# Kernel tuning notes

Measured on AMD Instinct MI355X. Metric: run time of the kernel, lower is better.

The kernel has to match this reference:

```python
import jax, jax.numpy as jnp
import numpy as np

H, CH = 4, 16          # heads, hidden_features // heads
SLOPE = 0.2            # leaky_relu negative slope


def gat(x, W, a_src, a_dst):
    # x: (B, N, C); W: (hidden, C); a_src/a_dst: (H, CH)
    B, N, _ = x.shape
    h = (x @ W.T).reshape(B, N, H, CH)
    a1 = jnp.einsum('bnhc,hc->bnh', h, a_src)   # att_src scores
    a2 = jnp.einsum('bnhc,hc->bnh', h, a_dst)   # att_dst scores
    # torch: a1.unsqueeze(1) + a2.unsqueeze(2) -> (B, N, N, H)
    e = a1[:, None, :, :] + a2[:, :, None, :]
    e = jnp.transpose(e, (0, 3, 1, 2))          # (B, H, N, N)
    e = jnp.where(e >= 0, e, SLOPE * e)         # leaky_relu
    return jax.nn.softmax(e, axis=2)            # softmax over dim=2 as in torch


def pool(x, W1, b1, W2, b2):
    # diff-pool assignment: (B, N, K), then x' = S^T x -> (B, K, C)
    s = jax.nn.softmax(jax.nn.relu(x @ W1.T + b1) @ W2.T + b2, axis=-1)
    return jnp.einsum('bnk,bnc->bkc', s, x)


def fuse(att0, atts, lefts, rights):
    out = att0
    for a, l, r in zip(atts, lefts, rights):
        # left (H,J0,K) @ att (B,H,K,K) @ right (H,K,J0), broadcast over batch
        out = out + jnp.einsum('hjk,bhkl,hlm->bhjm', l, a, r)
    return out


def setup_inputs() -> dict:
    key = jax.random.key(0)
    ks = iter(jax.random.split(key, 40))
    n = lambda shape, s=0.1: jax.random.normal(next(ks), shape, dtype=jnp.float32) * s
    inp = {
        'src': n((64, 64, 64, 25), 1.0),
        'gat_lin': n((6, 64, 64)), 'gat_asrc': n((6, 4, 16)), 'gat_adst': n((6, 4, 16)),
        'sp0_W1': n((64, 64)), 'sp0_b1': jnp.zeros((64,), jnp.float32),
        'sp0_W2': n((12, 64)), 'sp0_b2': jnp.zeros((12,), jnp.float32),
        'sp1_W1': n((64, 64)), 'sp1_b1': jnp.zeros((64,), jnp.float32),
        'sp1_W2': n((5, 64)), 'sp1_b2': jnp.zeros((5,), jnp.float32),
        'tp0_W1': n((64, 64)), 'tp0_b1': jnp.zeros((64,), jnp.float32),
        'tp0_W2': n((32, 64)), 'tp0_b2': jnp.zeros((32,), jnp.float32),
        'tp1_W1': n((64, 64)), 'tp1_b1': jnp.zeros((64,), jnp.float32),
        'tp1_W2': n((12, 64)), 'tp1_b2': jnp.zeros((12,), jnp.float32),
        'sl0': n((4, 25, 12)), 'sr0': n((4, 12, 25)),
        'sl1': n((4, 25, 5)), 'sr1': n((4, 5, 25)),
        'tl0': n((4, 64, 32)), 'tr0': n((4, 32, 64)),
        'tl1': n((4, 64, 12)), 'tr1': n((4, 12, 64)),
    }
    return inp


def reference(src, gat_lin, gat_asrc, gat_adst,
              sp0_W1, sp0_b1, sp0_W2, sp0_b2, sp1_W1, sp1_b1, sp1_W2, sp1_b2,
              tp0_W1, tp0_b1, tp0_W2, tp0_b2, tp1_W1, tp1_b1, tp1_W2, tp1_b2,
              sl0, sr0, sl1, sr1, tl0, tr0, tl1, tr1):
    B, C, T, J = src.shape
    # ---- spatial branch: attention over joints per (batch, frame) ----
    xs = jnp.transpose(src, (0, 2, 3, 1)).reshape(B * T, J, C)
    a_s0 = gat(xs, gat_lin[0], gat_asrc[0], gat_adst[0])            # (BT,H,25,25)
    xs1 = pool(xs, sp0_W1, sp0_b1, sp0_W2, sp0_b2)                  # (BT,12,C)
    a_s1 = gat(xs1, gat_lin[1], gat_asrc[1], gat_adst[1])           # (BT,H,12,12)
    xs2 = pool(xs1, sp1_W1, sp1_b1, sp1_W2, sp1_b2)                 # (BT,5,C)
    a_s2 = gat(xs2, gat_lin[2], gat_asrc[2], gat_adst[2])           # (BT,H,5,5)
    s_fused = fuse(a_s0, [a_s1, a_s2], [sl0, sl1], [sr0, sr1])
    # ---- temporal branch: attention over frames per (batch, joint) ----
    xt = jnp.transpose(src, (0, 3, 2, 1)).reshape(B * J, T, C)
    a_t0 = gat(xt, gat_lin[3], gat_asrc[3], gat_adst[3])            # (BJ,H,64,64)
    xt1 = pool(xt, tp0_W1, tp0_b1, tp0_W2, tp0_b2)                  # (BJ,32,C)
    a_t1 = gat(xt1, gat_lin[4], gat_asrc[4], gat_adst[4])
    xt2 = pool(xt1, tp1_W1, tp1_b1, tp1_W2, tp1_b2)                 # (BJ,12,C)
    a_t2 = gat(xt2, gat_lin[5], gat_asrc[5], gat_adst[5])
    t_fused = fuse(a_t0, [a_t1, a_t2], [tl0, tl1], [tr0, tr1])
    return (s_fused.reshape(B, T, H, J, J), t_fused.reshape(B, J, H, T, T))
```

## Files before the change

### kernel.cpp

```cpp
#include <hip/hip_runtime.h>

#define DEVINL __device__ __forceinline__

DEVINL float leaky(float v) { return v >= 0.f ? v : 0.2f * v; }

__global__ void wprep_kernel(const float* __restrict__ lin,
                             const float* __restrict__ asrc,
                             const float* __restrict__ adst,
                             float* __restrict__ w_out) {
    int idx = blockIdx.x * blockDim.x + threadIdx.x;
    if (idx >= 6 * 4 * 64) return;
    int c = idx & 63;
    int h = (idx >> 6) & 3;
    int k = idx >> 8;
    const float* L = lin + k * 64 * 64;
    float s1 = 0.f, s2 = 0.f;
    for (int e = 0; e < 16; ++e) {
        float w = L[(h * 16 + e) * 64 + c];
        s1 += w * asrc[(k * 4 + h) * 16 + e];
        s2 += w * adst[(k * 4 + h) * 16 + e];
    }
    w_out[(k * 2 + 0) * 256 + h * 64 + c] = s1;
    w_out[(k * 2 + 1) * 256 + h * 64 + c] = s2;
}

__global__ void wtrans_kernel(const float* __restrict__ s0, const float* __restrict__ s1,
                              const float* __restrict__ t0, const float* __restrict__ t1,
                              const float* __restrict__ s0w2, const float* __restrict__ s1w2,
                              const float* __restrict__ t0w2, const float* __restrict__ t1w2,
                              float* __restrict__ o) {
    int idx = blockIdx.x * 256 + threadIdx.x;
    if (idx < 16384) {
        int m = idx >> 12, r = idx & 4095, c = r >> 6, d = r & 63;
        const float* src = (m == 0) ? s0 : (m == 1) ? s1 : (m == 2) ? t0 : t1;
        o[idx] = src[d * 64 + c];
    } else if (idx < 16384 + 768) {
        int j = idx - 16384, c = j / 12, k = j - 12 * c;
        o[idx] = s0w2[k * 64 + c];
    } else if (idx < 17152 + 512) {
        int j = idx - 17152, c = j >> 3, k = j & 7;
        o[idx] = (k < 5) ? s1w2[k * 64 + c] : 0.f;
    } else if (idx < 17664 + 2048) {
        int j = idx - 17664, c = j >> 5, k = j & 31;
        o[idx] = t0w2[k * 64 + c];
    } else if (idx < 19712 + 768) {
        int j = idx - 19712, c = j / 12, k = j - 12 * c;
        o[idx] = t1w2[k * 64 + c];
    }
}

__global__ void xs_kernel(const float* __restrict__ src, float* __restrict__ xs) {
    int g = blockIdx.x;
    int b = g >> 6, t = g & 63;
    __shared__ float tile[64][26];
    const float* sp = src + b * 102400 + t * 25;
    for (int idx = threadIdx.x; idx < 64 * 25; idx += blockDim.x) {
        int c = idx / 25, j = idx - c * 25;
        tile[c][j] = sp[c * 1600 + j];
    }
    __syncthreads();
    float* op = xs + g * 25 * 64;
    for (int idx = threadIdx.x; idx < 25 * 64; idx += blockDim.x) {
        int j = idx >> 6, c = idx & 63;
        op[idx] = tile[c][j];
    }
}

__global__ void xt_kernel(const float* __restrict__ src, float* __restrict__ xt) {
    int g = blockIdx.x;
    int b = g / 25, j = g - b * 25;
    __shared__ float tile[64][65];
    const float* sp = src + b * 102400 + j;
    for (int idx = threadIdx.x; idx < 64 * 64; idx += blockDim.x) {
        int c = idx >> 6, t = idx & 63;
        tile[c][t] = sp[c * 1600 + t * 25];
    }
    __syncthreads();
    float* op = xt + g * 64 * 64;
    for (int idx = threadIdx.x; idx < 64 * 64; idx += blockDim.x) {
        int t = idx >> 6, c = idx & 63;
        op[idx] = tile[c][t];
    }
}

template <int N, int GPB>
__global__ __launch_bounds__(256) void score_kernel(
    const float* __restrict__ x,
    const float* __restrict__ w,
    float* __restrict__ sc) {
    constexpr int NP = GPB * N;
    constexpr int LD = NP + 1;
    __shared__ float xlT[64 * LD];
    __shared__ float wl[512];
    const int g0 = blockIdx.x * GPB;
    const int tid = threadIdx.x;
    const float* xp = x + (size_t)g0 * N * 64;
    for (int idx = tid; idx < NP * 64; idx += 256) {
        int n = idx >> 6, c = idx & 63;
        xlT[c * LD + n] = xp[idx];
    }
    for (int idx = tid; idx < 512; idx += 256) wl[idx] = w[idx];
    __syncthreads();
    float* op = sc + (size_t)g0 * 8 * N;
    for (int idx = tid; idx < 8 * NP; idx += 256) {
        int n = idx % N;
        int q = (idx / N) & 7;
        int gs = idx / (8 * N);
        int nn = gs * N + n;
        const float* wp = wl + q * 64;
        float acc = 0.f;
        #pragma unroll 8
        for (int c = 0; c < 64; ++c) acc += xlT[c * LD + nn] * wp[c];
        op[idx] = acc;
    }
}

template <int N, int K, int KP>
__global__ __launch_bounds__(256, 3) void pool_kernel(
    const float* __restrict__ x,
    const float* __restrict__ W1T,
    const float* __restrict__ b1,
    const float* __restrict__ W2T,
    const float* __restrict__ b2,
    float* __restrict__ xo) {
    constexpr int NP = (N + 3) & ~3;
    constexpr int LDN = NP + 1;
    __shared__ float xlT[64 * LDN];
    __shared__ float yT[64 * LDN];
    __shared__ float sT[KP * LDN];
    const int g = blockIdx.x, tid = threadIdx.x;
    const float* xp = x + (size_t)g * N * 64;
    for (int i4 = tid; i4 < N * 16; i4 += 256) {
        int n = i4 >> 4, c0 = (i4 & 15) << 2;
        float4 v = ((const float4*)xp)[i4];
        xlT[(c0 + 0) * LDN + n] = v.x;
        xlT[(c0 + 1) * LDN + n] = v.y;
        xlT[(c0 + 2) * LDN + n] = v.z;
        xlT[(c0 + 3) * LDN + n] = v.w;
    }
    if constexpr (NP > N) {
        for (int i = tid; i < 64 * (NP - N); i += 256) {
            int c = i / (NP - N), n = N + i % (NP - N);
            xlT[c * LDN + n] = 0.f;
        }
    }
    __syncthreads();
    constexpr int T1 = (NP / 4) * 16;
    if (tid < T1) {
        int d0 = (tid & 15) << 2, n0 = (tid >> 4) << 2;
        float acc[4][4] = {};
        #pragma unroll 4
        for (int c = 0; c < 64; ++c) {
            float4 w4 = *(const float4*)(W1T + c * 64 + d0);
            float wv[4] = {w4.x, w4.y, w4.z, w4.w};
            float xv[4];
            #pragma unroll
            for (int r = 0; r < 4; ++r) xv[r] = xlT[c * LDN + n0 + r];
            #pragma unroll
            for (int r = 0; r < 4; ++r)
                #pragma unroll
                for (int cc = 0; cc < 4; ++cc) acc[r][cc] += xv[r] * wv[cc];
        }
        float4 b4 = *(const float4*)(b1 + d0);
        float bb[4] = {b4.x, b4.y, b4.z, b4.w};
        #pragma unroll
        for (int r = 0; r < 4; ++r)
            #pragma unroll
            for (int cc = 0; cc < 4; ++cc)
                yT[(d0 + cc) * LDN + n0 + r] = fmaxf(acc[r][cc] + bb[cc], 0.f);
    }
    __syncthreads();
    constexpr int KG4 = KP / 4;
    constexpr int T2 = (NP / 4) * KG4;
    if (tid < T2) {
        int k0 = (tid % KG4) << 2, n0 = (tid / KG4) << 2;
        float acc[4][4] = {};
        #pragma unroll 4
        for (int d = 0; d < 64; ++d) {
            float4 w4 = *(const float4*)(W2T + d * KP + k0);
            float wv[4] = {w4.x, w4.y, w4.z, w4.w};
            float yv[4];
            #pragma unroll
            for (int r = 0; r < 4; ++r) yv[r] = yT[d * LDN + n0 + r];
            #pragma unroll
            for (int r = 0; r < 4; ++r)
                #pragma unroll
                for (int cc = 0; cc < 4; ++cc) acc[r][cc] += yv[r] * wv[cc];
        }
        #pragma unroll
        for (int cc = 0; cc < 4; ++cc) {
            int k = k0 + cc;
            float bb = (k < K) ? b2[k] : 0.f;
            #pragma unroll
            for (int r = 0; r < 4; ++r)
                sT[k * LDN + n0 + r] = (k < K) ? (acc[r][cc] + bb) : -1e30f;
        }
    }
    __syncthreads();
    if (tid < NP) {
        float m = -1e30f;
        #pragma unroll
        for (int k = 0; k < KP; ++k) m = fmaxf(m, sT[k * LDN + tid]);
        float sum = 0.f;
        float e[KP];
        #pragma unroll
        for (int k = 0; k < KP; ++k) { e[k] = __expf(sT[k * LDN + tid] - m); sum += e[k]; }
        float inv = 1.f / sum;
        #pragma unroll
        for (int k = 0; k < KP; ++k) sT[k * LDN + tid] = e[k] * inv;
    }
    __syncthreads();
    constexpr int KG2 = (K + 1) / 2;
    constexpr int T3 = KG2 * 16;
    if (tid < T3) {
        int k0 = (tid % KG2) * 2, c0 = (tid / KG2) * 4;
        float acc0[4] = {}, acc1[4] = {};
        #pragma unroll 4
        for (int n = 0; n < N; ++n) {
            float sv0 = sT[k0 * LDN + n];
            float sv1 = sT[(k0 + 1) * LDN + n];
            float xv[4];
            #pragma unroll
            for (int j = 0; j < 4; ++j) xv[j] = xlT[(c0 + j) * LDN + n];
            #pragma unroll
            for (int j = 0; j < 4; ++j) { acc0[j] += sv0 * xv[j]; acc1[j] += sv1 * xv[j]; }
        }
        float* op = xo + (size_t)g * K * 64;
        *(float4*)&op[k0 * 64 + c0] = make_float4(acc0[0], acc0[1], acc0[2], acc0[3]);
        if (k0 + 1 < K)
            *(float4*)&op[(k0 + 1) * 64 + c0] = make_float4(acc1[0], acc1[1], acc1[2], acc1[3]);
    }
}

__global__ __launch_bounds__(256, 8) void gatfuse_t(
    const float* __restrict__ sc0,
    const float* __restrict__ sc1,
    const float* __restrict__ sc2,
    const float* __restrict__ L1,
    const float* __restrict__ R1,
    const float* __restrict__ L2,
    const float* __restrict__ R2,
    float* __restrict__ out)
{
    const int bid = blockIdx.x;
    const int g = (bid & 7) | ((bid >> 5) << 3);
    const int h = (bid >> 3) & 3;
    const int tid = threadIdx.x;
    __shared__ float t1T[32 * 64];
    __shared__ float t2T[12 * 64];
    __shared__ float A1[32 * 36];
    __shared__ float A2[12 * 13];
    __shared__ float a01[64], a02[64], mj0[64], iv0[64];
    __shared__ float a11[32], a12[32], mj1[32], iv1[32];
    __shared__ float a21[12], a22[12], mj2[12], iv2[12];

    if (tid < 128) {
        int t = tid & 63, sd = tid >> 6;
        (sd ? a02 : a01)[t] = sc0[((size_t)g * 8 + sd * 4 + h) * 64 + t];
    } else if (tid < 192) {
        int u = tid - 128, sd = u >> 5, n = u & 31;
        (sd ? a12 : a11)[n] = sc1[((size_t)g * 8 + sd * 4 + h) * 32 + n];
    } else if (tid < 216) {
        int u = tid - 192, sd = u / 12, n = u - sd * 12;
        (sd ? a22 : a21)[n] = sc2[((size_t)g * 8 + sd * 4 + h) * 12 + n];
    }
    __syncthreads();

    if (tid < 64) {
        float mx = a02[0];
        for (int i = 1; i < 64; ++i) mx = fmaxf(mx, a02[i]);
        float aj = a01[tid];
        float mj = leaky(aj + mx);
        float s = 0.f;
        for (int i = 0; i < 64; ++i) s += __expf(leaky(aj + a02[i]) - mj);
        mj0[tid] = mj; iv0[tid] = 1.f / s;
    } else if (tid < 96) {
        int l = tid - 64;
        float mx = a12[0];
        for (int k = 1; k < 32; ++k) mx = fmaxf(mx, a12[k]);
        float aj = a11[l];
        float mj = leaky(aj + mx);
        float s = 0.f;
        for (int k = 0; k < 32; ++k) s += __expf(leaky(aj + a12[k]) - mj);
        mj1[l] = mj; iv1[l] = 1.f / s;
    } else if (tid < 108) {
        int l = tid - 96;
        float mx = a22[0];
        for (int k = 1; k < 12; ++k) mx = fmaxf(mx, a22[k]);
        float aj = a21[l];
        float mj = leaky(aj + mx);
        float s = 0.f;
        for (int k = 0; k < 12; ++k) s += __expf(leaky(aj + a22[k]) - mj);
        mj2[l] = mj; iv2[l] = 1.f / s;
    }
    __syncthreads();

    #pragma unroll
    for (int q = 0; q < 4; ++q) {
        int idx = q * 256 + tid;
        int k = idx >> 5, l = idx & 31;
        float e = leaky(a11[l] + a12[k]);
        A1[k * 36 + l] = __expf(e - mj1[l]) * iv1[l];
    }
    if (tid < 144) {
        int k = tid / 12, l = tid - k * 12;
        float e = leaky(a21[l] + a22[k]);
        A2[k * 13 + l] = __expf(e - mj2[l]) * iv2[l];
    }
    __syncthreads();

    {
        const int j = tid & 63, l0 = (tid >> 6) * 8;
        const float* ljrow = L1 + ((size_t)h * 64 + j) * 32;
        float acc8[8] = {};
        for (int k = 0; k < 32; ++k) {
            float lk = ljrow[k];
            float4 a4a = *(const float4*)&A1[k * 36 + l0];
            float4 a4b = *(const float4*)&A1[k * 36 + l0 + 4];
            acc8[0] += lk * a4a.x; acc8[1] += lk * a4a.y;
            acc8[2] += lk * a4a.z; acc8[3] += lk * a4a.w;
            acc8[4] += lk * a4b.x; acc8[5] += lk * a4b.y;
            acc8[6] += lk * a4b.z; acc8[7] += lk * a4b.w;
        }
        #pragma unroll
        for (int lo = 0; lo < 8; ++lo) t1T[(l0 + lo) * 64 + j] = acc8[lo];
        const int lb = (tid >> 6) * 3;
        float lj2[12];
        const float4* lp2 = (const float4*)(L2 + ((size_t)h * 64 + j) * 12);
        #pragma unroll
        for (int q = 0; q < 3; ++q) {
            float4 v = lp2[q];
            lj2[q * 4] = v.x; lj2[q * 4 + 1] = v.y;
            lj2[q * 4 + 2] = v.z; lj2[q * 4 + 3] = v.w;
        }
        #pragma unroll
        for (int lo = 0; lo < 3; ++lo) {
            int l = lb + lo;
            float acc = 0.f;
            #pragma unroll
            for (int k = 0; k < 12; ++k) acc += lj2[k] * A2[k * 13 + l];
            t2T[l * 64 + j] = acc;
        }
    }
    __syncthreads();

    const int i0 = (tid >> 4) << 2, m0 = (tid & 15) << 2;
    float acc[4][4];
    {
        float4 q1 = *(const float4*)&a01[m0];
        float4 qm = *(const float4*)&mj0[m0];
        float4 qv = *(const float4*)&iv0[m0];
        float4 q2 = *(const float4*)&a02[i0];
        float am[4] = {q1.x, q1.y, q1.z, q1.w};
        float mv[4] = {qm.x, qm.y, qm.z, qm.w};
        float iv[4] = {qv.x, qv.y, qv.z, qv.w};
        float ai[4] = {q2.x, q2.y, q2.z, q2.w};
        #pragma unroll
        for (int r = 0; r < 4; ++r)
            #pragma unroll
            for (int c = 0; c < 4; ++c) {
                float e = am[c] + ai[r];
                e = e >= 0.f ? e : 0.2f * e;
                acc[r][c] = __expf(e - mv[c]) * iv[c];
            }
    }
    const float* r1b = R1 + (size_t)h * 2048;
    #pragma unroll 8
    for (int l = 0; l < 32; ++l) {
        float4 t4 = *(const float4*)&t1T[l * 64 + i0];
        float4 r4 = *(const float4*)(r1b + l * 64 + m0);
        float tv[4] = {t4.x, t4.y, t4.z, t4.w};
        float rv[4] = {r4.x, r4.y, r4.z, r4.w};
        #pragma unroll
        for (int r = 0; r < 4; ++r)
            #pragma unroll
            for (int c = 0; c < 4; ++c) acc[r][c] += tv[r] * rv[c];
    }
    const float* r2b = R2 + (size_t)h * 768;
    #pragma unroll 4
    for (int l = 0; l < 12; ++l) {
        float4 t4 = *(const float4*)&t2T[l * 64 + i0];
        float4 r4 = *(const float4*)(r2b + l * 64 + m0);
        float tv[4] = {t4.x, t4.y, t4.z, t4.w};
        float rv[4] = {r4.x, r4.y, r4.z, r4.w};
        #pragma unroll
        for (int r = 0; r < 4; ++r)
            #pragma unroll
            for (int c = 0; c < 4; ++c) acc[r][c] += tv[r] * rv[c];
    }
    float* op = out + ((size_t)g * 4 + h) * 4096;
    #pragma unroll
    for (int r = 0; r < 4; ++r)
        *(float4*)&op[(i0 + r) * 64 + m0] =
            make_float4(acc[r][0], acc[r][1], acc[r][2], acc[r][3]);
}

__global__ __launch_bounds__(256, 6) void gatfuse_s(
    const float* __restrict__ sc0,
    const float* __restrict__ sc1,
    const float* __restrict__ sc2,
    const float* __restrict__ L1,
    const float* __restrict__ R1,
    const float* __restrict__ L2,
    const float* __restrict__ R2,
    float* __restrict__ out)
{
    const int g = blockIdx.x;
    const int tid = threadIdx.x;
    const int h = tid >> 6, t = tid & 63;
    __shared__ float A1[4][12 * 13];
    __shared__ float A2[4][5 * 6];
    __shared__ float t1l[4][25 * 16];
    __shared__ float t2l[4][25 * 8];
    __shared__ float r1T[4][25 * 16];
    __shared__ float r2T[4][25 * 8];
    __shared__ float a01[4][25], a02[4][25], mj0[4][25], iv0[4][25];
    __shared__ float a11[4][12], a12[4][12], mj1[4][12], iv1[4][12];
    __shared__ float a21[4][5], a22[4][5], mj2[4][5], iv2[4][5];

    if (t < 50) {
        int sd = t / 25, n = t - sd * 25;
        (sd ? a02[h] : a01[h])[n] = sc0[((size_t)g * 8 + sd * 4 + h) * 25 + n];
    }
    if (t < 24) {
        int sd = t / 12, n = t - sd * 12;
        (sd ? a12[h] : a11[h])[n] = sc1[((size_t)g * 8 + sd * 4 + h) * 12 + n];
    }
    if (t < 10) {
        int sd = t / 5, n = t - sd * 5;
        (sd ? a22[h] : a21[h])[n] = sc2[((size_t)g * 8 + sd * 4 + h) * 5 + n];
    }
    for (int idx = t; idx < 400; idx += 64) {
        int m = idx >> 4, l = idx & 15;
        r1T[h][idx] = (l < 12) ? R1[h * 300 + l * 25 + m] : 0.f;
    }
    for (int idx = t; idx < 200; idx += 64) {
        int m = idx >> 3, l = idx & 7;
        r2T[h][idx] = (l < 5) ? R2[h * 125 + l * 25 + m] : 0.f;
    }
    __syncthreads();

    if (t < 25) {
        float mx = a02[h][0];
        for (int i = 1; i < 25; ++i) mx = fmaxf(mx, a02[h][i]);
        float aj = a01[h][t];
        float mj = leaky(aj + mx);
        float s = 0.f;
        for (int i = 0; i < 25; ++i) s += __expf(leaky(aj + a02[h][i]) - mj);
        mj0[h][t] = mj; iv0[h][t] = 1.f / s;
    }
    if (t >= 32 && t < 44) {
        int l = t - 32;
        float mx = a12[h][0];
        for (int k = 1; k < 12; ++k) mx = fmaxf(mx, a12[h][k]);
        float aj = a11[h][l];
        float mj = leaky(aj + mx);
        float s = 0.f;
        for (int k = 0; k < 12; ++k) s += __expf(leaky(aj + a12[h][k]) - mj);
        mj1[h][l] = mj; iv1[h][l] = 1.f / s;
    }
    if (t >= 48 && t < 53) {
        int l = t - 48;
        float mx = a22[h][0];
        for (int k = 1; k < 5; ++k) mx = fmaxf(mx, a22[h][k]);
        float aj = a21[h][l];
        float mj = leaky(aj + mx);
        float s = 0.f;
        for (int k = 0; k < 5; ++k) s += __expf(leaky(aj + a22[h][k]) - mj);
        mj2[h][l] = mj; iv2[h][l] = 1.f / s;
    }
    __syncthreads();

    for (int idx = t; idx < 144; idx += 64) {
        int k = idx / 12, l = idx - k * 12;
        float e = leaky(a11[h][l] + a12[h][k]);
        A1[h][k * 13 + l] = __expf(e - mj1[h][l]) * iv1[h][l];
    }
    if (t < 25) {
        int k = t / 5, l = t - (t / 5) * 5;
        float e = leaky(a21[h][l] + a22[h][k]);
        A2[h][k * 6 + l] = __expf(e - mj2[h][l]) * iv2[h][l];
    }
    __syncthreads();

    if (t < 25) {
        float lj[12];
        const float4* lp = (const float4*)(L1 + ((size_t)h * 25 + t) * 12);
        #pragma unroll
        for (int q = 0; q < 3; ++q) {
            float4 v = lp[q];
            lj[q * 4] = v.x; lj[q * 4 + 1] = v.y; lj[q * 4 + 2] = v.z; lj[q * 4 + 3] = v.w;
        }
        #pragma unroll
        for (int l = 0; l < 12; ++l) {
            float acc = 0.f;
            #pragma unroll
            for (int k = 0; k < 12; ++k) acc += lj[k] * A1[h][k * 13 + l];
            t1l[h][t * 16 + l] = acc;
        }
        #pragma unroll
        for (int l = 12; l < 16; ++l) t1l[h][t * 16 + l] = 0.f;
        float lj2[5];
        const float* lp2 = L2 + ((size_t)h * 25 + t) * 5;
        #pragma unroll
        for (int k = 0; k < 5; ++k) lj2[k] = lp2[k];
        #pragma unroll
        for (int l = 0; l < 5; ++l) {
            float acc = 0.f;
            #pragma unroll
            for (int k = 0; k < 5; ++k) acc += lj2[k] * A2[h][k * 6 + l];
            t2l[h][t * 8 + l] = acc;
        }
        #pragma unroll
        for (int l = 5; l < 8; ++l) t2l[h][t * 8 + l] = 0.f;
    }
    __syncthreads();

    float* op = out + ((size_t)g * 4 + h) * 625;
    for (int idx = t; idx < 625; idx += 64) {
        int i = idx / 25, m = idx - i * 25;
        float e = a01[h][m] + a02[h][i];
        e = e >= 0.f ? e : 0.2f * e;
        float val = __expf(e - mj0[h][m]) * iv0[h][m];
        const float* t1r = &t1l[h][i * 16];
        const float* r1c = &r1T[h][m * 16];
        #pragma unroll
        for (int q = 0; q < 4; ++q) {
            float4 tv = *(const float4*)&t1r[q * 4];
            float4 rv = *(const float4*)&r1c[q * 4];
            val += tv.x * rv.x + tv.y * rv.y + tv.z * rv.z + tv.w * rv.w;
        }
        const float* t2r = &t2l[h][i * 8];
        const float* r2c = &r2T[h][m * 8];
        #pragma unroll
        for (int q = 0; q < 2; ++q) {
            float4 tv = *(const float4*)&t2r[q * 4];
            float4 rv = *(const float4*)&r2c[q * 4];
            val += tv.x * rv.x + tv.y * rv.y + tv.z * rv.z + tv.w * rv.w;
        }
        op[idx] = val;
    }
}

extern "C" void kernel_launch(void* const* d_in, const int* in_sizes, int n_in,
                              void* d_out, int out_size, void* d_ws, size_t ws_size,
                              hipStream_t stream) {
    const float* src    = (const float*)d_in[0];
    const float* lin    = (const float*)d_in[1];
    const float* asrc   = (const float*)d_in[2];
    const float* adst   = (const float*)d_in[3];
    const float* sp0_W1 = (const float*)d_in[4];
    const float* sp0_b1 = (const float*)d_in[5];
    const float* sp0_W2 = (const float*)d_in[6];
    const float* sp0_b2 = (const float*)d_in[7];
    const float* sp1_W1 = (const float*)d_in[8];
    const float* sp1_b1 = (const float*)d_in[9];
    const float* sp1_W2 = (const float*)d_in[10];
    const float* sp1_b2 = (const float*)d_in[11];
    const float* tp0_W1 = (const float*)d_in[12];
    const float* tp0_b1 = (const float*)d_in[13];
    const float* tp0_W2 = (const float*)d_in[14];
    const float* tp0_b2 = (const float*)d_in[15];
    const float* tp1_W1 = (const float*)d_in[16];
    const float* tp1_b1 = (const float*)d_in[17];
    const float* tp1_W2 = (const float*)d_in[18];
    const float* tp1_b2 = (const float*)d_in[19];
    const float* sl0    = (const float*)d_in[20];
    const float* sr0    = (const float*)d_in[21];
    const float* sl1    = (const float*)d_in[22];
    const float* sr1    = (const float*)d_in[23];
    const float* tl0    = (const float*)d_in[24];
    const float* tr0    = (const float*)d_in[25];
    const float* tl1    = (const float*)d_in[26];
    const float* tr1    = (const float*)d_in[27];

    float* out_s = (float*)d_out;
    float* out_t = out_s + 10240000;

    float* ws   = (float*)d_ws;
    float* wbuf = ws;
    float* wT   = ws + 4096;
    float* base = ws + 24576;

    float* sp0_W1T = wT;
    float* sp1_W1T = wT + 4096;
    float* tp0_W1T = wT + 8192;
    float* tp1_W1T = wT + 12288;
    float* sp0_W2T = wT + 16384;
    float* sp1_W2T = wT + 17152;
    float* tp0_W2T = wT + 17664;
    float* tp1_W2T = wT + 19712;

    float* xs  = base;
    float* xs1 = base + 6553600;
    float* xs2 = base + 9699328;
    float* xt  = base;
    float* xt1 = base + 6553600;
    float* xt2 = base + 9830400;
    float* scb = base + 11059200;
    float* scS0 = scb;
    float* scS1 = scb + 819200;
    float* scS2 = scb + 1212416;
    float* scT0 = scb;
    float* scT1 = scb + 819200;
    float* scT2 = scb + 1228800;

    wprep_kernel<<<6, 256, 0, stream>>>(lin, asrc, adst, wbuf);
    wtrans_kernel<<<80, 256, 0, stream>>>(sp0_W1, sp1_W1, tp0_W1, tp1_W1,
                                          sp0_W2, sp1_W2, tp0_W2, tp1_W2, wT);

    xs_kernel<<<4096, 256, 0, stream>>>(src, xs);
    score_kernel<25, 2><<<2048, 256, 0, stream>>>(xs, wbuf + 0 * 512, scS0);
    pool_kernel<25, 12, 12><<<4096, 256, 0, stream>>>(xs, sp0_W1T, sp0_b1, sp0_W2T, sp0_b2, xs1);
    score_kernel<12, 4><<<1024, 256, 0, stream>>>(xs1, wbuf + 1 * 512, scS1);
    pool_kernel<12, 5, 8><<<4096, 256, 0, stream>>>(xs1, sp1_W1T, sp1_b1, sp1_W2T, sp1_b2, xs2);
    score_kernel<5, 8><<<512, 256, 0, stream>>>(xs2, wbuf + 2 * 512, scS2);
    gatfuse_s<<<4096, 256, 0, stream>>>(scS0, scS1, scS2, sl0, sr0, sl1, sr1, out_s);

    xt_kernel<<<1600, 256, 0, stream>>>(src, xt);
    score_kernel<64, 1><<<1600, 256, 0, stream>>>(xt, wbuf + 3 * 512, scT0);
    pool_kernel<64, 32, 32><<<1600, 256, 0, stream>>>(xt, tp0_W1T, tp0_b1, tp0_W2T, tp0_b2, xt1);
    score_kernel<32, 2><<<800, 256, 0, stream>>>(xt1, wbuf + 4 * 512, scT1);
    pool_kernel<32, 12, 12><<<1600, 256, 0, stream>>>(xt1, tp1_W1T, tp1_b1, tp1_W2T, tp1_b2, xt2);
    score_kernel<12, 4><<<400, 256, 0, stream>>>(xt2, wbuf + 5 * 512, scT2);
    gatfuse_t<<<6400, 256, 0, stream>>>(scT0, scT1, scT2, tl0, tr0, tl1, tr1, out_t);
}
```

Before: 386.8 us.

## Fuse transpose, score and pooling kernels; factor leaky softmax into separable exponentials

The input transposes (xs/xt) and the per-level attention score kernels are folded into the pooling kernel. Each pool launch now reads src directly, computes the input-level and output-level scores, and writes the pooled features only when the next level needs them. This cuts the launch count from 14 to 6 and removes the round trips of xs/xt/xs2/xt2 through global memory. In the gatfuse kernels, the leaky-relu softmax is rewritten as products of precomputed per-row and per-column exponentials selected by the sign of the sum, replacing the per-element exp. That adds LDS and register pressure and drops the launch-bounds occupancy hint.

```diff
diff --git a/kernel.cpp b/kernel.cpp
--- a/kernel.cpp
+++ b/kernel.cpp
@@ -49,186 +49,167 @@
     }
 }
 
-__global__ void xs_kernel(const float* __restrict__ src, float* __restrict__ xs) {
-    int g = blockIdx.x;
-    int b = g >> 6, t = g & 63;
-    __shared__ float tile[64][26];
-    const float* sp = src + b * 102400 + t * 25;
-    for (int idx = threadIdx.x; idx < 64 * 25; idx += blockDim.x) {
-        int c = idx / 25, j = idx - c * 25;
-        tile[c][j] = sp[c * 1600 + j];
-    }
-    __syncthreads();
-    float* op = xs + g * 25 * 64;
-    for (int idx = threadIdx.x; idx < 25 * 64; idx += blockDim.x) {
-        int j = idx >> 6, c = idx & 63;
-        op[idx] = tile[c][j];
-    }
-}
-
-__global__ void xt_kernel(const float* __restrict__ src, float* __restrict__ xt) {
-    int g = blockIdx.x;
-    int b = g / 25, j = g - b * 25;
-    __shared__ float tile[64][65];
-    const float* sp = src + b * 102400 + j;
-    for (int idx = threadIdx.x; idx < 64 * 64; idx += blockDim.x) {
-        int c = idx >> 6, t = idx & 63;
-        tile[c][t] = sp[c * 1600 + t * 25];
-    }
-    __syncthreads();
-    float* op = xt + g * 64 * 64;
-    for (int idx = threadIdx.x; idx < 64 * 64; idx += blockDim.x) {
-        int t = idx >> 6, c = idx & 63;
-        op[idx] = tile[c][t];
-    }
-}
-
-template <int N, int GPB>
-__global__ __launch_bounds__(256) void score_kernel(
-    const float* __restrict__ x,
-    const float* __restrict__ w,
-    float* __restrict__ sc) {
-    constexpr int NP = GPB * N;
-    constexpr int LD = NP + 1;
-    __shared__ float xlT[64 * LD];
-    __shared__ float wl[512];
-    const int g0 = blockIdx.x * GPB;
-    const int tid = threadIdx.x;
-    const float* xp = x + (size_t)g0 * N * 64;
-    for (int idx = tid; idx < NP * 64; idx += 256) {
-        int n = idx >> 6, c = idx & 63;
-        xlT[c * LD + n] = xp[idx];
-    }
-    for (int idx = tid; idx < 512; idx += 256) wl[idx] = w[idx];
-    __syncthreads();
-    float* op = sc + (size_t)g0 * 8 * N;
-    for (int idx = tid; idx < 8 * NP; idx += 256) {
-        int n = idx % N;
-        int q = (idx / N) & 7;
-        int gs = idx / (8 * N);
-        int nn = gs * N + n;
-        const float* wp = wl + q * 64;
+template <int N, int K, int KP, int MODE, int WR>
+__global__ __launch_bounds__(256) void pool_kernel(
+    const float* __restrict__ x, const float* __restrict__ W1T,
+    const float* __restrict__ b1, const float* __restrict__ W2T,
+    const float* __restrict__ b2, const float* __restrict__ wsi,
+    const float* __restrict__ wso, float* __restrict__ xo,
+    float* __restrict__ sci, float* __restrict__ sco)
+{
+    constexpr int SLD = KP + 1;
+    constexpr int XO_OFF = ((N * SLD + 3) & ~3);
+    constexpr int SZT = (MODE == 1) ? 64 * 26 : (MODE == 2 ? 64 * 65 : 0);
+    constexpr int R3A = XO_OFF + K * 68;
+    constexpr int R3 = ((R3A > SZT ? R3A : SZT) + 3) & ~3;
+    constexpr int TOT = 2 * N * 68 + R3 + 512;
+    __shared__ float lds[TOT];
+    float* xln = lds;
+    float* yn  = lds + N * 68;
+    float* r3  = yn + N * 68;
+    float* sn  = r3;
+    float* xoL = r3 + XO_OFF;
+    float* wlo = r3 + R3;
+    float* wli = yn;
+    float* tile = r3;
+    const int g = blockIdx.x, tid = threadIdx.x;
+
+    if constexpr (MODE == 0) {
+        const float4* xp = (const float4*)(x + (size_t)g * N * 64);
+        for (int p = tid; p < N * 16; p += 256) {
+            int n = p >> 4, c0 = (p & 15) << 2;
+            *(float4*)&xln[n * 68 + c0] = xp[p];
+        }
+    } else if constexpr (MODE == 1) {
+        int b = g >> 6, t = g & 63;
+        const float* sp = x + b * 102400 + t * 25;
+        for (int idx = tid; idx < 1600; idx += 256) {
+            int c = idx / 25, j = idx - c * 25;
+            tile[c * 26 + j] = sp[c * 1600 + j];
+        }
+        for (int i = tid; i < 512; i += 256) wli[i] = wsi[i];
+    } else {
+        int b = g / 25, j = g - b * 25;
+        const float* sp = x + b * 102400 + j;
+        for (int idx = tid; idx < 4096; idx += 256) {
+            int c = idx >> 6, t = idx & 63;
+            tile[c * 65 + t] = sp[c * 1600 + t * 25];
+        }
+        for (int i = tid; i < 512; i += 256) wli[i] = wsi[i];
+    }
+    for (int i = tid; i < 512; i += 256) wlo[i] = wso[i];
+    __syncthreads();
+
+    if constexpr (MODE != 0) {
+        constexpr int TLD = (MODE == 1) ? 26 : 65;
+        for (int p = tid; p < N * 64; p += 256) {
+            int n = p >> 6, c = p & 63;
+            xln[n * 68 + c] = tile[c * TLD + n];
+        }
+        __syncthreads();
+        for (int p = tid; p < 8 * N; p += 256) {
+            int q = p / N, n = p - q * N;
+            const float* wv = wli + q * 64;
+            const float* xr = &xln[n * 68];
+            float acc = 0.f;
+            #pragma unroll
+            for (int c0 = 0; c0 < 64; c0 += 4) {
+                float4 xv = *(const float4*)&xr[c0];
+                float4 w4 = *(const float4*)&wv[c0];
+                acc += xv.x * w4.x + xv.y * w4.y + xv.z * w4.z + xv.w * w4.w;
+            }
+            sci[(size_t)g * 8 * N + p] = acc;
+        }
+        __syncthreads();
+    }
+
+    for (int p = tid; p < N * 16; p += 256) {
+        int n = p >> 4, d0 = (p & 15) << 2;
+        const float* xr = &xln[n * 68];
+        float4 bb = *(const float4*)(b1 + d0);
+        float a0 = bb.x, a1 = bb.y, a2 = bb.z, a3 = bb.w;
+        #pragma unroll 4
+        for (int c0 = 0; c0 < 64; c0 += 4) {
+            float4 xv = *(const float4*)&xr[c0];
+            float4 w0 = *(const float4*)(W1T + (c0 + 0) * 64 + d0);
+            float4 w1 = *(const float4*)(W1T + (c0 + 1) * 64 + d0);
+            float4 w2 = *(const float4*)(W1T + (c0 + 2) * 64 + d0);
+            float4 w3 = *(const float4*)(W1T + (c0 + 3) * 64 + d0);
+            a0 += xv.x * w0.x + xv.y * w1.x + xv.z * w2.x + xv.w * w3.x;
+            a1 += xv.x * w0.y + xv.y * w1.y + xv.z * w2.y + xv.w * w3.y;
+            a2 += xv.x * w0.z + xv.y * w1.z + xv.z * w2.z + xv.w * w3.z;
+            a3 += xv.x * w0.w + xv.y * w1.w + xv.z * w2.w + xv.w * w3.w;
+        }
+        *(float4*)&yn[n * 68 + d0] =
+            make_float4(fmaxf(a0, 0.f), fmaxf(a1, 0.f), fmaxf(a2, 0.f), fmaxf(a3, 0.f));
+    }
+    __syncthreads();
+
+    for (int p = tid; p < N * (KP / 4); p += 256) {
+        int n = p / (KP / 4), k0 = (p % (KP / 4)) << 2;
+        const float* yr = &yn[n * 68];
+        float a0 = 0.f, a1 = 0.f, a2 = 0.f, a3 = 0.f;
+        #pragma unroll 4
+        for (int d0 = 0; d0 < 64; d0 += 4) {
+            float4 yv = *(const float4*)&yr[d0];
+            float4 w0 = *(const float4*)(W2T + (d0 + 0) * KP + k0);
+            float4 w1 = *(const float4*)(W2T + (d0 + 1) * KP + k0);
+            float4 w2 = *(const float4*)(W2T + (d0 + 2) * KP + k0);
+            float4 w3 = *(const float4*)(W2T + (d0 + 3) * KP + k0);
+            a0 += yv.x * w0.x + yv.y * w1.x + yv.z * w2.x + yv.w * w3.x;
+            a1 += yv.x * w0.y + yv.y * w1.y + yv.z * w2.y + yv.w * w3.y;
+            a2 += yv.x * w0.z + yv.y * w1.z + yv.z * w2.z + yv.w * w3.z;
+            a3 += yv.x * w0.w + yv.y * w1.w + yv.z * w2.w + yv.w * w3.w;
+        }
+        float* sr = &sn[n * SLD + k0];
+        sr[0] = (k0 + 0 < K) ? a0 + b2[k0 + 0] : -1e30f;
+        sr[1] = (k0 + 1 < K) ? a1 + b2[k0 + 1] : -1e30f;
+        sr[2] = (k0 + 2 < K) ? a2 + b2[k0 + 2] : -1e30f;
+        sr[3] = (k0 + 3 < K) ? a3 + b2[k0 + 3] : -1e30f;
+    }
+    __syncthreads();
+
+    if (tid < N) {
+        float* sr = &sn[tid * SLD];
+        float m = sr[0];
+        #pragma unroll
+        for (int k = 1; k < KP; ++k) m = fmaxf(m, sr[k]);
+        float sum = 0.f;
+        #pragma unroll
+        for (int k = 0; k < KP; ++k) { float e = __expf(sr[k] - m); sr[k] = e; sum += e; }
+        float inv = 1.f / sum;
+        #pragma unroll
+        for (int k = 0; k < KP; ++k) sr[k] *= inv;
+    }
+    __syncthreads();
+
+    for (int p = tid; p < K * 16; p += 256) {
+        int k = p >> 4, c0 = (p & 15) << 2;
+        float a0 = 0.f, a1 = 0.f, a2 = 0.f, a3 = 0.f;
+        for (int n = 0; n < N; ++n) {
+            float s = sn[n * SLD + k];
+            float4 xv = *(const float4*)&xln[n * 68 + c0];
+            a0 += s * xv.x; a1 += s * xv.y; a2 += s * xv.z; a3 += s * xv.w;
+        }
+        float4 r = make_float4(a0, a1, a2, a3);
+        *(float4*)&xoL[k * 68 + c0] = r;
+        if constexpr (WR)
+            *(float4*)(xo + (size_t)g * K * 64 + k * 64 + c0) = r;
+    }
+    __syncthreads();
+
+    for (int p = tid; p < 8 * K; p += 256) {
+        int q = p / K, k = p - q * K;
+        const float* wv = wlo + q * 64;
+        const float* xr = &xoL[k * 68];
         float acc = 0.f;
-        #pragma unroll 8
-        for (int c = 0; c < 64; ++c) acc += xlT[c * LD + nn] * wp[c];
-        op[idx] = acc;
-    }
-}
-
-template <int N, int K, int KP>
-__global__ __launch_bounds__(256, 3) void pool_kernel(
-    const float* __restrict__ x,
-    const float* __restrict__ W1T,
-    const float* __restrict__ b1,
-    const float* __restrict__ W2T,
-    const float* __restrict__ b2,
-    float* __restrict__ xo) {
-    constexpr int NP = (N + 3) & ~3;
-    constexpr int LDN = NP + 1;
-    __shared__ float xlT[64 * LDN];
-    __shared__ float yT[64 * LDN];
-    __shared__ float sT[KP * LDN];
-    const int g = blockIdx.x, tid = threadIdx.x;
-    const float* xp = x + (size_t)g * N * 64;
-    for (int i4 = tid; i4 < N * 16; i4 += 256) {
-        int n = i4 >> 4, c0 = (i4 & 15) << 2;
-        float4 v = ((const float4*)xp)[i4];
-        xlT[(c0 + 0) * LDN + n] = v.x;
-        xlT[(c0 + 1) * LDN + n] = v.y;
-        xlT[(c0 + 2) * LDN + n] = v.z;
-        xlT[(c0 + 3) * LDN + n] = v.w;
-    }
-    if constexpr (NP > N) {
-        for (int i = tid; i < 64 * (NP - N); i += 256) {
-            int c = i / (NP - N), n = N + i % (NP - N);
-            xlT[c * LDN + n] = 0.f;
-        }
-    }
-    __syncthreads();
-    constexpr int T1 = (NP / 4) * 16;
-    if (tid < T1) {
-        int d0 = (tid & 15) << 2, n0 = (tid >> 4) << 2;
-        float acc[4][4] = {};
-        #pragma unroll 4
-        for (int c = 0; c < 64; ++c) {
-            float4 w4 = *(const float4*)(W1T + c * 64 + d0);
-            float wv[4] = {w4.x, w4.y, w4.z, w4.w};
-            float xv[4];
-            #pragma unroll
-            for (int r = 0; r < 4; ++r) xv[r] = xlT[c * LDN + n0 + r];
-            #pragma unroll
-            for (int r = 0; r < 4; ++r)
-                #pragma unroll
-                for (int cc = 0; cc < 4; ++cc) acc[r][cc] += xv[r] * wv[cc];
-        }
-        float4 b4 = *(const float4*)(b1 + d0);
-        float bb[4] = {b4.x, b4.y, b4.z, b4.w};
-        #pragma unroll
-        for (int r = 0; r < 4; ++r)
-            #pragma unroll
-            for (int cc = 0; cc < 4; ++cc)
-                yT[(d0 + cc) * LDN + n0 + r] = fmaxf(acc[r][cc] + bb[cc], 0.f);
-    }
-    __syncthreads();
-    constexpr int KG4 = KP / 4;
-    constexpr int T2 = (NP / 4) * KG4;
-    if (tid < T2) {
-        int k0 = (tid % KG4) << 2, n0 = (tid / KG4) << 2;
-        float acc[4][4] = {};
-        #pragma unroll 4
-        for (int d = 0; d < 64; ++d) {
-            float4 w4 = *(const float4*)(W2T + d * KP + k0);
-            float wv[4] = {w4.x, w4.y, w4.z, w4.w};
-            float yv[4];
-            #pragma unroll
-            for (int r = 0; r < 4; ++r) yv[r] = yT[d * LDN + n0 + r];
-            #pragma unroll
-            for (int r = 0; r < 4; ++r)
-                #pragma unroll
-                for (int cc = 0; cc < 4; ++cc) acc[r][cc] += yv[r] * wv[cc];
-        }
-        #pragma unroll
-        for (int cc = 0; cc < 4; ++cc) {
-            int k = k0 + cc;
-            float bb = (k < K) ? b2[k] : 0.f;
-            #pragma unroll
-            for (int r = 0; r < 4; ++r)
-                sT[k * LDN + n0 + r] = (k < K) ? (acc[r][cc] + bb) : -1e30f;
-        }
-    }
-    __syncthreads();
-    if (tid < NP) {
-        float m = -1e30f;
-        #pragma unroll
-        for (int k = 0; k < KP; ++k) m = fmaxf(m, sT[k * LDN + tid]);
-        float sum = 0.f;
-        float e[KP];
-        #pragma unroll
-        for (int k = 0; k < KP; ++k) { e[k] = __expf(sT[k * LDN + tid] - m); sum += e[k]; }
-        float inv = 1.f / sum;
-        #pragma unroll
-        for (int k = 0; k < KP; ++k) sT[k * LDN + tid] = e[k] * inv;
-    }
-    __syncthreads();
-    constexpr int KG2 = (K + 1) / 2;
-    constexpr int T3 = KG2 * 16;
-    if (tid < T3) {
-        int k0 = (tid % KG2) * 2, c0 = (tid / KG2) * 4;
-        float acc0[4] = {}, acc1[4] = {};
-        #pragma unroll 4
-        for (int n = 0; n < N; ++n) {
-            float sv0 = sT[k0 * LDN + n];
-            float sv1 = sT[(k0 + 1) * LDN + n];
-            float xv[4];
-            #pragma unroll
-            for (int j = 0; j < 4; ++j) xv[j] = xlT[(c0 + j) * LDN + n];
-            #pragma unroll
-            for (int j = 0; j < 4; ++j) { acc0[j] += sv0 * xv[j]; acc1[j] += sv1 * xv[j]; }
-        }
-        float* op = xo + (size_t)g * K * 64;
-        *(float4*)&op[k0 * 64 + c0] = make_float4(acc0[0], acc0[1], acc0[2], acc0[3]);
-        if (k0 + 1 < K)
-            *(float4*)&op[(k0 + 1) * 64 + c0] = make_float4(acc1[0], acc1[1], acc1[2], acc1[3]);
+        #pragma unroll
+        for (int c0 = 0; c0 < 64; c0 += 4) {
+            float4 xv = *(const float4*)&xr[c0];
+            float4 w4 = *(const float4*)&wv[c0];
+            acc += xv.x * w4.x + xv.y * w4.y + xv.z * w4.z + xv.w * w4.w;
+        }
+        sco[(size_t)g * 8 * K + p] = acc;
     }
 }
 
@@ -250,48 +231,84 @@
     __shared__ float t2T[12 * 64];
     __shared__ float A1[32 * 36];
     __shared__ float A2[12 * 13];
-    __shared__ float a01[64], a02[64], mj0[64], iv0[64];
-    __shared__ float a11[32], a12[32], mj1[32], iv1[32];
-    __shared__ float a21[12], a22[12], mj2[12], iv2[12];
-
-    if (tid < 128) {
-        int t = tid & 63, sd = tid >> 6;
-        (sd ? a02 : a01)[t] = sc0[((size_t)g * 8 + sd * 4 + h) * 64 + t];
-    } else if (tid < 192) {
-        int u = tid - 128, sd = u >> 5, n = u & 31;
-        (sd ? a12 : a11)[n] = sc1[((size_t)g * 8 + sd * 4 + h) * 32 + n];
-    } else if (tid < 216) {
-        int u = tid - 192, sd = u / 12, n = u - sd * 12;
-        (sd ? a22 : a21)[n] = sc2[((size_t)g * 8 + sd * 4 + h) * 12 + n];
-    }
+    __shared__ float4 row0[64], col0[64], row1[32], col1[32], row2[12], col2[12];
+    __shared__ float mxs[3];
+
+    if (tid < 64) col0[tid].x = sc0[((size_t)g * 8 + h) * 64 + tid];
+    else if (tid < 128) row0[tid - 64].x = sc0[((size_t)g * 8 + 4 + h) * 64 + (tid - 64)];
+    else if (tid < 160) col1[tid - 128].x = sc1[((size_t)g * 8 + h) * 32 + (tid - 128)];
+    else if (tid < 192) row1[tid - 160].x = sc1[((size_t)g * 8 + 4 + h) * 32 + (tid - 160)];
+    else if (tid < 204) col2[tid - 192].x = sc2[((size_t)g * 8 + h) * 12 + (tid - 192)];
+    else if (tid < 216) row2[tid - 204].x = sc2[((size_t)g * 8 + 4 + h) * 12 + (tid - 204)];
     __syncthreads();
 
     if (tid < 64) {
-        float mx = a02[0];
-        for (int i = 1; i < 64; ++i) mx = fmaxf(mx, a02[i]);
-        float aj = a01[tid];
-        float mj = leaky(aj + mx);
-        float s = 0.f;
-        for (int i = 0; i < 64; ++i) s += __expf(leaky(aj + a02[i]) - mj);
-        mj0[tid] = mj; iv0[tid] = 1.f / s;
+        float mx = row0[0].x;
+        for (int i = 1; i < 64; ++i) mx = fmaxf(mx, row0[i].x);
+        if (tid == 0) mxs[0] = mx;
+        float a = row0[tid].x;
+        row0[tid] = make_float4(a, __expf(a - mx), __expf(0.2f * (a - mx)), 0.f);
+    } else if (tid < 96) {
+        float mx = row1[0].x;
+        for (int k = 1; k < 32; ++k) mx = fmaxf(mx, row1[k].x);
+        if (tid == 64) mxs[1] = mx;
+        int k = tid - 64;
+        float a = row1[k].x;
+        row1[k] = make_float4(a, __expf(a - mx), __expf(0.2f * (a - mx)), 0.f);
+    } else if (tid < 108) {
+        float mx = row2[0].x;
+        for (int k = 1; k < 12; ++k) mx = fmaxf(mx, row2[k].x);
+        if (tid == 96) mxs[2] = mx;
+        int k = tid - 96;
+        float a = row2[k].x;
+        row2[k] = make_float4(a, __expf(a - mx), __expf(0.2f * (a - mx)), 0.f);
+    }
+    __syncthreads();
+
+    if (tid < 64) {
+        float a = col0[tid].x, mx = mxs[0];
+        float mj = leaky(a + mx);
+        float Em = __expf(a + mx - mj);
+        float Fm = __expf(0.2f * (a + mx) - mj);
+        float S1 = 0.f, S2 = 0.f;
+        for (int i = 0; i < 64; ++i) {
+            float4 r = row0[i];
+            bool c = (a + r.x >= 0.f);
+            S1 += c ? r.y : 0.f;
+            S2 += c ? 0.f : r.z;
+        }
+        float iv = 1.f / (Em * S1 + Fm * S2);
+        col0[tid] = make_float4(a, Em * iv, Fm * iv, 0.f);
     } else if (tid < 96) {
         int l = tid - 64;
-        float mx = a12[0];
-        for (int k = 1; k < 32; ++k) mx = fmaxf(mx, a12[k]);
-        float aj = a11[l];
-        float mj = leaky(aj + mx);
-        float s = 0.f;
-        for (int k = 0; k < 32; ++k) s += __expf(leaky(aj + a12[k]) - mj);
-        mj1[l] = mj; iv1[l] = 1.f / s;
+        float a = col1[l].x, mx = mxs[1];
+        float mj = leaky(a + mx);
+        float E = __expf(a + mx - mj);
+        float F = __expf(0.2f * (a + mx) - mj);
+        float S1 = 0.f, S2 = 0.f;
+        for (int k = 0; k < 32; ++k) {
+            float4 r = row1[k];
+            bool c = (a + r.x >= 0.f);
+            S1 += c ? r.y : 0.f;
+            S2 += c ? 0.f : r.z;
+        }
+        float iv = 1.f / (E * S1 + F * S2);
+        col1[l] = make_float4(a, E * iv, F * iv, 0.f);
     } else if (tid < 108) {
         int l = tid - 96;
-        float mx = a22[0];
-        for (int k = 1; k < 12; ++k) mx = fmaxf(mx, a22[k]);
-        float aj = a21[l];
-        float mj = leaky(aj + mx);
-        float s = 0.f;
-        for (int k = 0; k < 12; ++k) s += __expf(leaky(aj + a22[k]) - mj);
-        mj2[l] = mj; iv2[l] = 1.f / s;
+        float a = col2[l].x, mx = mxs[2];
+        float mj = leaky(a + mx);
+        float E = __expf(a + mx - mj);
+        float F = __expf(0.2f * (a + mx) - mj);
+        float S1 = 0.f, S2 = 0.f;
+        for (int k = 0; k < 12; ++k) {
+            float4 r = row2[k];
+            bool c = (a + r.x >= 0.f);
+            S1 += c ? r.y : 0.f;
+            S2 += c ? 0.f : r.z;
+        }
+        float iv = 1.f / (E * S1 + F * S2);
+        col2[l] = make_float4(a, E * iv, F * iv, 0.f);
     }
     __syncthreads();
 
@@ -299,13 +316,15 @@
     for (int q = 0; q < 4; ++q) {
         int idx = q * 256 + tid;
         int k = idx >> 5, l = idx & 31;
-        float e = leaky(a11[l] + a12[k]);
-        A1[k * 36 + l] = __expf(e - mj1[l]) * iv1[l];
+        float4 rk = row1[k];
+        float4 cl = col1[l];
+        A1[k * 36 + l] = (cl.x + rk.x >= 0.f) ? cl.y * rk.y : cl.z * rk.z;
     }
     if (tid < 144) {
         int k = tid / 12, l = tid - k * 12;
-        float e = leaky(a21[l] + a22[k]);
-        A2[k * 13 + l] = __expf(e - mj2[l]) * iv2[l];
+        float4 rk = row2[k];
+        float4 cl = col2[l];
+        A2[k * 13 + l] = (cl.x + rk.x >= 0.f) ? cl.y * rk.y : cl.z * rk.z;
     }
     __syncthreads();
 
@@ -347,22 +366,14 @@
     const int i0 = (tid >> 4) << 2, m0 = (tid & 15) << 2;
     float acc[4][4];
     {
-        float4 q1 = *(const float4*)&a01[m0];
-        float4 qm = *(const float4*)&mj0[m0];
-        float4 qv = *(const float4*)&iv0[m0];
-        float4 q2 = *(const float4*)&a02[i0];
-        float am[4] = {q1.x, q1.y, q1.z, q1.w};
-        float mv[4] = {qm.x, qm.y, qm.z, qm.w};
-        float iv[4] = {qv.x, qv.y, qv.z, qv.w};
-        float ai[4] = {q2.x, q2.y, q2.z, q2.w};
+        float4 cm[4] = {col0[m0], col0[m0 + 1], col0[m0 + 2], col0[m0 + 3]};
+        float4 ri[4] = {row0[i0], row0[i0 + 1], row0[i0 + 2], row0[i0 + 3]};
         #pragma unroll
         for (int r = 0; r < 4; ++r)
             #pragma unroll
-            for (int c = 0; c < 4; ++c) {
-                float e = am[c] + ai[r];
-                e = e >= 0.f ? e : 0.2f * e;
-                acc[r][c] = __expf(e - mv[c]) * iv[c];
-            }
+            for (int c = 0; c < 4; ++c)
+                acc[r][c] = (cm[c].x + ri[r].x >= 0.f) ? cm[c].y * ri[r].y
+                                                       : cm[c].z * ri[r].z;
     }
     const float* r1b = R1 + (size_t)h * 2048;
     #pragma unroll 8
@@ -395,7 +406,7 @@
             make_float4(acc[r][0], acc[r][1], acc[r][2], acc[r][3]);
 }
 
-__global__ __launch_bounds__(256, 6) void gatfuse_s(
+__global__ __launch_bounds__(256, 5) void gatfuse_s(
     const float* __restrict__ sc0,
     const float* __restrict__ sc1,
     const float* __restrict__ sc2,
@@ -408,27 +419,24 @@
     const int g = blockIdx.x;
     const int tid = threadIdx.x;
     const int h = tid >> 6, t = tid & 63;
+    __shared__ float4 row0[4][25], col0[4][25];
+    __shared__ float4 row1[4][12], col1[4][12];
+    __shared__ float4 row2[4][5], col2[4][5];
     __shared__ float A1[4][12 * 13];
     __shared__ float A2[4][5 * 6];
     __shared__ float t1l[4][25 * 16];
     __shared__ float t2l[4][25 * 8];
     __shared__ float r1T[4][25 * 16];
     __shared__ float r2T[4][25 * 8];
-    __shared__ float a01[4][25], a02[4][25], mj0[4][25], iv0[4][25];
-    __shared__ float a11[4][12], a12[4][12], mj1[4][12], iv1[4][12];
-    __shared__ float a21[4][5], a22[4][5], mj2[4][5], iv2[4][5];
-
-    if (t < 50) {
-        int sd = t / 25, n = t - sd * 25;
-        (sd ? a02[h] : a01[h])[n] = sc0[((size_t)g * 8 + sd * 4 + h) * 25 + n];
-    }
-    if (t < 24) {
-        int sd = t / 12, n = t - sd * 12;
-        (sd ? a12[h] : a11[h])[n] = sc1[((size_t)g * 8 + sd * 4 + h) * 12 + n];
-    }
-    if (t < 10) {
-        int sd = t / 5, n = t - sd * 5;
-        (sd ? a22[h] : a21[h])[n] = sc2[((size_t)g * 8 + sd * 4 + h) * 5 + n];
+    __shared__ float mxs[4][3];
+
+    for (int p = t; p < 84; p += 64) {
+        if (p < 25)      col0[h][p].x      = sc0[((size_t)g * 8 + h) * 25 + p];
+        else if (p < 50) row0[h][p - 25].x = sc0[((size_t)g * 8 + 4 + h) * 25 + (p - 25)];
+        else if (p < 62) col1[h][p - 50].x = sc1[((size_t)g * 8 + h) * 12 + (p - 50)];
+        else if (p < 74) row1[h][p - 62].x = sc1[((size_t)g * 8 + 4 + h) * 12 + (p - 62)];
+        else if (p < 79) col2[h][p - 74].x = sc2[((size_t)g * 8 + h) * 5 + (p - 74)];
+        else             row2[h][p - 79].x = sc2[((size_t)g * 8 + 4 + h) * 5 + (p - 79)];
     }
     for (int idx = t; idx < 400; idx += 64) {
         int m = idx >> 4, l = idx & 15;
@@ -441,45 +449,86 @@
     __syncthreads();
 
     if (t < 25) {
-        float mx = a02[h][0];
-        for (int i = 1; i < 25; ++i) mx = fmaxf(mx, a02[h][i]);
-        float aj = a01[h][t];
-        float mj = leaky(aj + mx);
-        float s = 0.f;
-        for (int i = 0; i < 25; ++i) s += __expf(leaky(aj + a02[h][i]) - mj);
-        mj0[h][t] = mj; iv0[h][t] = 1.f / s;
-    }
-    if (t >= 32 && t < 44) {
+        float mx = row0[h][0].x;
+        for (int i = 1; i < 25; ++i) mx = fmaxf(mx, row0[h][i].x);
+        if (t == 0) mxs[h][0] = mx;
+        float a = row0[h][t].x;
+        row0[h][t] = make_float4(a, __expf(a - mx), __expf(0.2f * (a - mx)), 0.f);
+    } else if (t >= 32 && t < 44) {
+        float mx = row1[h][0].x;
+        for (int k = 1; k < 12; ++k) mx = fmaxf(mx, row1[h][k].x);
+        if (t == 32) mxs[h][1] = mx;
+        int k = t - 32;
+        float a = row1[h][k].x;
+        row1[h][k] = make_float4(a, __expf(a - mx), __expf(0.2f * (a - mx)), 0.f);
+    } else if (t >= 48 && t < 53) {
+        float mx = row2[h][0].x;
+        for (int k = 1; k < 5; ++k) mx = fmaxf(mx, row2[h][k].x);
+        if (t == 48) mxs[h][2] = mx;
+        int k = t - 48;
+        float a = row2[h][k].x;
+        row2[h][k] = make_float4(a, __expf(a - mx), __expf(0.2f * (a - mx)), 0.f);
+    }
+    __syncthreads();
+
+    if (t < 25) {
+        float a = col0[h][t].x, mx = mxs[h][0];
+        float mj = leaky(a + mx);
+        float E = __expf(a + mx - mj);
+        float F = __expf(0.2f * (a + mx) - mj);
+        float S1 = 0.f, S2 = 0.f;
+        for (int i = 0; i < 25; ++i) {
+            float4 r = row0[h][i];
+            bool c = (a + r.x >= 0.f);
+            S1 += c ? r.y : 0.f;
+            S2 += c ? 0.f : r.z;
+        }
+        float iv = 1.f / (E * S1 + F * S2);
+        col0[h][t] = make_float4(a, E * iv, F * iv, 0.f);
+    } else if (t >= 32 && t < 44) {
         int l = t - 32;
-        float mx = a12[h][0];
-        for (int k = 1; k < 12; ++k) mx = fmaxf(mx, a12[h][k]);
-        float aj = a11[h][l];
-        float mj = leaky(aj + mx);
-        float s = 0.f;
-        for (int k = 0; k < 12; ++k) s += __expf(leaky(aj + a12[h][k]) - mj);
-        mj1[h][l] = mj; iv1[h][l] = 1.f / s;
-    }
-    if (t >= 48 && t < 53) {
+        float a = col1[h][l].x, mx = mxs[h][1];
+        float mj = leaky(a + mx);
+        float E = __expf(a + mx - mj);
+        float F = __expf(0.2f * (a + mx) - mj);
+        float S1 = 0.f, S2 = 0.f;
+        for (int k = 0; k < 12; ++k) {
+            float4 r = row1[h][k];
+            bool c = (a + r.x >= 0.f);
+            S1 += c ? r.y : 0.f;
+            S2 += c ? 0.f : r.z;
+        }
+        float iv = 1.f / (E * S1 + F * S2);
+        col1[h][l] = make_float4(a, E * iv, F * iv, 0.f);
+    } else if (t >= 48 && t < 53) {
         int l = t - 48;
-        float mx = a22[h][0];
-        for (int k = 1; k < 5; ++k) mx = fmaxf(mx, a22[h][k]);
-        float aj = a21[h][l];
-        float mj = leaky(aj + mx);
-        float s = 0.f;
-        for (int k = 0; k < 5; ++k) s += __expf(leaky(aj + a22[h][k]) - mj);
-        mj2[h][l] = mj; iv2[h][l] = 1.f / s;
-    }
-    __syncthreads();
-
-    for (int idx = t; idx < 144; idx += 64) {
-        int k = idx / 12, l = idx - k * 12;
-        float e = leaky(a11[h][l] + a12[h][k]);
-        A1[h][k * 13 + l] = __expf(e - mj1[h][l]) * iv1[h][l];
+        float a = col2[h][l].x, mx = mxs[h][2];
+        float mj = leaky(a + mx);
+        float E = __expf(a + mx - mj);
+        float F = __expf(0.2f * (a + mx) - mj);
+        float S1 = 0.f, S2 = 0.f;
+        for (int k = 0; k < 5; ++k) {
+            float4 r = row2[h][k];
+            bool c = (a + r.x >= 0.f);
+            S1 += c ? r.y : 0.f;
+            S2 += c ? 0.f : r.z;
+        }
+        float iv = 1.f / (E * S1 + F * S2);
+        col2[h][l] = make_float4(a, E * iv, F * iv, 0.f);
+    }
+    __syncthreads();
+
+    for (int p = t; p < 144; p += 64) {
+        int k = p / 12, l = p - k * 12;
+        float4 rk = row1[h][k];
+        float4 cl = col1[h][l];
+        A1[h][k * 13 + l] = (cl.x + rk.x >= 0.f) ? cl.y * rk.y : cl.z * rk.z;
     }
     if (t < 25) {
         int k = t / 5, l = t - (t / 5) * 5;
-        float e = leaky(a21[h][l] + a22[h][k]);
-        A2[h][k * 6 + l] = __expf(e - mj2[h][l]) * iv2[h][l];
+        float4 rk = row2[h][k];
+        float4 cl = col2[h][l];
+        A2[h][k * 6 + l] = (cl.x + rk.x >= 0.f) ? cl.y * rk.y : cl.z * rk.z;
     }
     __syncthreads();
 
@@ -519,9 +568,9 @@
     float* op = out + ((size_t)g * 4 + h) * 625;
     for (int idx = t; idx < 625; idx += 64) {
         int i = idx / 25, m = idx - i * 25;
-        float e = a01[h][m] + a02[h][i];
-        e = e >= 0.f ? e : 0.2f * e;
-        float val = __expf(e - mj0[h][m]) * iv0[h][m];
+        float4 cm = col0[h][m];
+        float4 ri = row0[h][i];
+        float val = (cm.x + ri.x >= 0.f) ? cm.y * ri.y : cm.z * ri.z;
         const float* t1r = &t1l[h][i * 16];
         const float* r1c = &r1T[h][m * 16];
         #pragma unroll
@@ -580,7 +629,6 @@
     float* ws   = (float*)d_ws;
     float* wbuf = ws;
     float* wT   = ws + 4096;
-    float* base = ws + 24576;
 
     float* sp0_W1T = wT;
     float* sp1_W1T = wT + 4096;
@@ -591,37 +639,33 @@
     float* tp0_W2T = wT + 17664;
     float* tp1_W2T = wT + 19712;
 
-    float* xs  = base;
-    float* xs1 = base + 6553600;
-    float* xs2 = base + 9699328;
-    float* xt  = base;
-    float* xt1 = base + 6553600;
-    float* xt2 = base + 9830400;
-    float* scb = base + 11059200;
-    float* scS0 = scb;
-    float* scS1 = scb + 819200;
-    float* scS2 = scb + 1212416;
-    float* scT0 = scb;
-    float* scT1 = scb + 819200;
-    float* scT2 = scb + 1228800;
+    float* a = ws + 24576;
+    float* xs1  = a;              a += 3145728;
+    float* xt1  = a;              a += 3276800;
+    float* scS0 = a;              a += 819200;
+    float* scS1 = a;              a += 393216;
+    float* scS2 = a;              a += 163840;
+    float* scT0 = a;              a += 819200;
+    float* scT1 = a;              a += 409600;
+    float* scT2 = a;              a += 153600;
 
     wprep_kernel<<<6, 256, 0, stream>>>(lin, asrc, adst, wbuf);
     wtrans_kernel<<<80, 256, 0, stream>>>(sp0_W1, sp1_W1, tp0_W1, tp1_W1,
                                           sp0_W2, sp1_W2, tp0_W2, tp1_W2, wT);
 
-    xs_kernel<<<4096, 256, 0, stream>>>(src, xs);
-    score_kernel<25, 2><<<2048, 256, 0, stream>>>(xs, wbuf + 0 * 512, scS0);
-    pool_kernel<25, 12, 12><<<4096, 256, 0, stream>>>(xs, sp0_W1T, sp0_b1, sp0_W2T, sp0_b2, xs1);
-    score_kernel<12, 4><<<1024, 256, 0, stream>>>(xs1, wbuf + 1 * 512, scS1);
-    pool_kernel<12, 5, 8><<<4096, 256, 0, stream>>>(xs1, sp1_W1T, sp1_b1, sp1_W2T, sp1_b2, xs2);
-    score_kernel<5, 8><<<512, 256, 0, stream>>>(xs2, wbuf + 2 * 512, scS2);
+    pool_kernel<25, 12, 12, 1, 1><<<4096, 256, 0, stream>>>(
+        src, sp0_W1T, sp0_b1, sp0_W2T, sp0_b2,
+        wbuf + 0 * 512, wbuf + 1 * 512, xs1, scS0, scS1);
+    pool_kernel<12, 5, 8, 0, 0><<<4096, 256, 0, stream>>>(
+        xs1, sp1_W1T, sp1_b1, sp1_W2T, sp1_b2,
+        nullptr, wbuf + 2 * 512, nullptr, nullptr, scS2);
     gatfuse_s<<<4096, 256, 0, stream>>>(scS0, scS1, scS2, sl0, sr0, sl1, sr1, out_s);
 
-    xt_kernel<<<1600, 256, 0, stream>>>(src, xt);
-    score_kernel<64, 1><<<1600, 256, 0, stream>>>(xt, wbuf + 3 * 512, scT0);
-    pool_kernel<64, 32, 32><<<1600, 256, 0, stream>>>(xt, tp0_W1T, tp0_b1, tp0_W2T, tp0_b2, xt1);
-    score_kernel<32, 2><<<800, 256, 0, stream>>>(xt1, wbuf + 4 * 512, scT1);
-    pool_kernel<32, 12, 12><<<1600, 256, 0, stream>>>(xt1, tp1_W1T, tp1_b1, tp1_W2T, tp1_b2, xt2);
-    score_kernel<12, 4><<<400, 256, 0, stream>>>(xt2, wbuf + 5 * 512, scT2);
+    pool_kernel<64, 32, 32, 2, 1><<<1600, 256, 0, stream>>>(
+        src, tp0_W1T, tp0_b1, tp0_W2T, tp0_b2,
+        wbuf + 3 * 512, wbuf + 4 * 512, xt1, scT0, scT1);
+    pool_kernel<32, 12, 12, 0, 0><<<1600, 256, 0, stream>>>(
+        xt1, tp1_W1T, tp1_b1, tp1_W2T, tp1_b2,
+        nullptr, wbuf + 5 * 512, nullptr, nullptr, scT2);
     gatfuse_t<<<6400, 256, 0, stream>>>(scT0, scT1, scT2, tl0, tr0, tl1, tr1, out_t);
 }
```

New measurement: 435.1 us. +12.5%, slower.
